# Performance work log

Hardware: AMD Instinct MI355X
Metric: run time of the kernel (lower is better)

Reference implementation:

```python
import jax, jax.numpy as jnp
import numpy as np

D_IN = 1024
D_OUT = 1024
NUM_HEADS = 16
HEAD_DIM = D_OUT // NUM_HEADS


def setup_inputs() -> dict:
    key = jax.random.key(0)
    ks = jax.random.split(key, 6)
    s = 0.02
    x = jax.random.normal(ks[0], (2, 2048, D_IN), dtype=jnp.float32)
    wq = jax.random.normal(ks[1], (D_IN, D_OUT), dtype=jnp.float32) * s
    wk = jax.random.normal(ks[2], (D_IN, D_OUT), dtype=jnp.float32) * s
    wv = jax.random.normal(ks[3], (D_IN, D_OUT), dtype=jnp.float32) * s
    wo = jax.random.normal(ks[4], (D_OUT, D_OUT), dtype=jnp.float32) * s
    bo = jax.random.normal(ks[5], (D_OUT,), dtype=jnp.float32) * s
    return {"x": x, "wq": wq, "wk": wk, "wv": wv, "wo": wo, "bo": bo}


def reference(x, wq, wk, wv, wo, bo):
    B, S, _ = x.shape
    # QKV projections (no bias, qkv_bias=False)
    def split_heads(t):
        return t.reshape(B, S, NUM_HEADS, HEAD_DIM).transpose(0, 2, 1, 3)  # [B,H,S,Dh]
    q = split_heads(x @ wq)
    k = split_heads(x @ wk)
    v = split_heads(x @ wv)
    scores = jnp.einsum('bhqd,bhkd->bhqk', q, k) / np.sqrt(HEAD_DIM).astype(np.float32)
    causal = jnp.tril(jnp.ones((S, S), dtype=bool))  # [S,S]
    scores = jnp.where(causal[None, None], scores, -jnp.inf)
    attn = jax.nn.softmax(scores, axis=-1)  # dropout p=0.0 -> identity
    ctx = jnp.einsum('bhqk,bhkd->bhqd', attn, v)
    ctx = ctx.transpose(0, 2, 1, 3).reshape(B, S, D_OUT)
    return ctx @ wo + bo
```

## Files before the change

kernel.cpp:

```cpp
#include <hip/hip_runtime.h>

typedef short s16x8 __attribute__((ext_vector_type(8)));
typedef float f32x4 __attribute__((ext_vector_type(4)));
typedef float f32x16 __attribute__((ext_vector_type(16)));
typedef unsigned int u32;
typedef u32 u32x2 __attribute__((ext_vector_type(2)));
typedef u32 u32x4 __attribute__((ext_vector_type(4)));
typedef unsigned short u16;

#define MFMA16(a, b, c) __builtin_amdgcn_mfma_f32_16x16x32_bf16((a), (b), (c), 0, 0, 0)
#define MFMA32(a, b, c) __builtin_amdgcn_mfma_f32_32x32x16_bf16((a), (b), (c), 0, 0, 0)

__device__ __forceinline__ u16 f2bf(float f) {
  unsigned u = __builtin_bit_cast(unsigned, f);
  unsigned r = (u + 0x7FFFu + ((u >> 16) & 1u)) >> 16;
  return (u16)r;
}

__device__ __forceinline__ u32 pack2bf(float lo, float hi) {
  return (u32)f2bf(lo) | ((u32)f2bf(hi) << 16);
}

__device__ __forceinline__ u32 cvtpk(float lo, float hi) {
  u32 r;
  asm("v_cvt_pk_bf16_f32 %0, %1, %2" : "=v"(r) : "v"(lo), "v"(hi));
  return r;
}

__device__ __forceinline__ float bf2f(u32 lo16) {
  return __builtin_bit_cast(float, lo16 << 16);
}

__device__ __forceinline__ void gl_lds16(const u16* g, u16* s) {
  __builtin_amdgcn_global_load_lds(
      (const __attribute__((address_space(1))) void*)g,
      (__attribute__((address_space(3))) void*)s, 16, 0, 0);
}

__global__ __launch_bounds__(256) void cvt_bf16(const float* __restrict__ in,
                                                u16* __restrict__ out, int n4) {
  int i = blockIdx.x * 256 + threadIdx.x;
  if (i < n4) {
    float4 v = reinterpret_cast<const float4*>(in)[i];
    ushort4 o;
    o.x = f2bf(v.x); o.y = f2bf(v.y); o.z = f2bf(v.z); o.w = f2bf(v.w);
    reinterpret_cast<ushort4*>(out)[i] = o;
  }
}

__global__ __launch_bounds__(256) void transp4(const float* __restrict__ wq,
                                               const float* __restrict__ wk,
                                               const float* __restrict__ wv,
                                               const float* __restrict__ wo,
                                               u16* __restrict__ wqkvt,
                                               u16* __restrict__ wot, float qscale) {
  __shared__ float tile[64][65];
  int z = blockIdx.z;
  const float* W = (z == 0) ? wq : (z == 1) ? wk : (z == 2) ? wv : wo;
  u16* out = (z < 3) ? (wqkvt + z * 1048576) : wot;
  float sc = (z == 0) ? qscale : 1.0f;
  int n0 = blockIdx.x * 64, k0 = blockIdx.y * 64;
  int t = threadIdx.x;
#pragma unroll
  for (int i = 0; i < 16; i++) {
    int idx = t + i * 256;
    int r = idx >> 6, c = idx & 63;
    tile[r][c] = W[(k0 + r) * 1024 + (n0 + c)];
  }
  __syncthreads();
#pragma unroll
  for (int i = 0; i < 16; i++) {
    int idx = t + i * 256;
    int r = idx >> 6, c = idx & 63;
    out[(n0 + r) * 1024 + (k0 + c)] = f2bf(tile[c][r] * sc);
  }
}

template <int MODE>
__global__ __launch_bounds__(256) void gemm2(const u16* __restrict__ A,
                                             const u16* __restrict__ Bt,
                                             const float* __restrict__ bias,
                                             void* __restrict__ outp) {
  constexpr int K = 1024, NT = K / 32;
  __shared__ __align__(16) u16 As[2][128 * 32];
  __shared__ __align__(16) u16 Bs[2][128 * 32];
  int t = threadIdx.x, w = t >> 6, l = t & 63;
  int m0 = blockIdx.y * 128, n0 = blockIdx.x * 128;
  int wm = (w >> 1) * 64, wn = (w & 1) * 64;
  int g = l >> 4, ql = l & 15;

  f32x4 acc[4][4];
#pragma unroll
  for (int i = 0; i < 4; i++)
#pragma unroll
    for (int j = 0; j < 4; j++) acc[i][j] = f32x4{0.f, 0.f, 0.f, 0.f};

  int lrow = l >> 2, lcol = (l & 3) * 8;
  const u16* Ag0 = A + (m0 + 32 * w + lrow) * K + lcol;
  const u16* Bg0 = Bt + (n0 + 32 * w + lrow) * K + lcol;
  u16* Asw[2] = {&As[0][(32 * w) * 32], &As[1][(32 * w) * 32]};
  u16* Bsw[2] = {&Bs[0][(32 * w) * 32], &Bs[1][(32 * w) * 32]};

#define STAGE(buf, kt)                              \
  do {                                              \
    int k0_ = (kt) * 32;                            \
    gl_lds16(Ag0 + k0_, Asw[buf]);                  \
    gl_lds16(Ag0 + 16 * K + k0_, Asw[buf] + 512);   \
    gl_lds16(Bg0 + k0_, Bsw[buf]);                  \
    gl_lds16(Bg0 + 16 * K + k0_, Bsw[buf] + 512);   \
  } while (0)

#define COMPUTE(buf)                                                              \
  do {                                                                            \
    s16x8 af[4], bv[4];                                                           \
    _Pragma("unroll") for (int fm = 0; fm < 4; fm++)                              \
        af[fm] = *reinterpret_cast<const s16x8*>(                                 \
            &As[buf][(wm + fm * 16 + ql) * 32 + g * 8]);                          \
    _Pragma("unroll") for (int fn = 0; fn < 4; fn++)                              \
        bv[fn] = *reinterpret_cast<const s16x8*>(                                 \
            &Bs[buf][(wn + fn * 16 + ql) * 32 + g * 8]);                          \
    _Pragma("unroll") for (int fm = 0; fm < 4; fm++)                              \
        _Pragma("unroll") for (int fn = 0; fn < 4; fn++)                          \
            acc[fm][fn] = MFMA16(af[fm], bv[fn], acc[fm][fn]);                    \
  } while (0)

  STAGE(0, 0);
  __syncthreads();
  int cur = 0;
  for (int kt = 0; kt < NT - 1; kt++) {
    STAGE(cur ^ 1, kt + 1);
    COMPUTE(cur);
    __syncthreads();
    cur ^= 1;
  }
  COMPUTE(cur);
#undef STAGE
#undef COMPUTE

#pragma unroll
  for (int fm = 0; fm < 4; fm++)
#pragma unroll
    for (int fn = 0; fn < 4; fn++)
#pragma unroll
      for (int j = 0; j < 4; j++) {
        int m = m0 + wm + fm * 16 + g * 4 + j;
        int n = n0 + wn + fn * 16 + ql;
        float v = acc[fm][fn][j];
        if (MODE == 0) {
          int proj = n >> 10, nn = n & 1023;
          int bh = (m >> 11) * 16 + (nn >> 6);
          int hd = nn & 63, srow = m & 2047;
          u16* o = (u16*)outp + proj * 4194304;
          if (proj < 2) {
            o[(bh * 2048 + srow) * 64 + hd] = f2bf(v);
          } else {
            int sp = (srow & ~12) | ((srow & 4) << 1) | ((srow & 8) >> 1);
            o[(bh * 64 + hd) * 2048 + sp] = f2bf(v);
          }
        } else {
          ((float*)outp)[m * 1024 + n] = v + bias[n];
        }
      }
}

__global__ __launch_bounds__(512, 4) void attn_kernel(const u16* __restrict__ Q,
                                                      const u16* __restrict__ Kb,
                                                      const u16* __restrict__ Vt,
                                                      u16* __restrict__ Ctx,
                                                      u16* __restrict__ part_o,
                                                      float* __restrict__ part_l) {
  __shared__ __align__(16) u16 Kl[2][2048];
  __shared__ __align__(16) u16 Vl[2][2048];
  __shared__ __align__(16) u16 tl[8][32 * 68];
  int tid = threadIdx.x, w = tid >> 6, l = tid & 63;
  int lq = l & 31, h = l >> 5;

  int B = blockIdx.x;
  int head = (B & 7) + 8 * ((B >> 3) & 3);
  int u = B >> 5;
  const signed char QCv[16] = {3, 2, 4, 4, 6, 6, 6, 7, 7, 7, 7, 5, 5, 5, 1, 0};
  const signed char CKv[16] = {0, 0, 0, 1, 0, 1, 2, 0, 1, 2, 3, 0, 1, 2, 0, 0};
  int qc = QCv[u], ck = CKv[u];
  int t0, t1;
  if (qc == 4)      { t0 = ck * 20; t1 = t0 + 20; }
  else if (qc == 5) { t0 = ck * 16; t1 = t0 + 16; }
  else if (qc == 6) { t0 = (ck == 0) ? 0 : (ck == 1) ? 19 : 38;
                      t1 = (ck == 0) ? 19 : (ck == 1) ? 38 : 56; }
  else if (qc == 7) { t0 = ck * 16; t1 = t0 + 16; }
  else              { t0 = 0; t1 = (qc + 1) * 8; }
  int dtile = qc * 8 + w;
  int q0w = qc * 256 + w * 32;
  int q = q0w + lq;

  const u16* Qp = Q + (head * 2048 + q0w) * 64;
  const u16* Kp = Kb + head * 2048 * 64;
  const u16* Vp = Vt + head * 64 * 2048;

  s16x8 qf[4];
#pragma unroll
  for (int f = 0; f < 4; f++)
    qf[f] = *reinterpret_cast<const s16x8*>(Qp + lq * 64 + f * 16 + h * 8);

  const u16* gstage;
  int gstep, ldsoff;
  if (w < 4) {
    int row = w * 8 + (l >> 3);
    int c = (l & 7) ^ (row & 7);
    gstage = Kp + row * 64 + c * 8;
    gstep = 32 * 64;
    ldsoff = w * 512;
  } else {
    int lin = (w - 4) * 64 + l;
    int rp = lin >> 3, pos = lin & 7;
    int d = rp * 2 + (pos >> 2);
    int c = (pos & 3) ^ (rp & 3);
    gstage = Vp + d * 2048 + c * 8;
    gstep = 32;
    ldsoff = (w - 4) * 512;
  }

  f32x16 oacc[2];
#pragma unroll
  for (int dt = 0; dt < 2; dt++)
#pragma unroll
    for (int rr = 0; rr < 16; rr++) oacc[dt][rr] = 0.f;
  float lsum = 0.f;

#define STAGE(buf, kt)                                                    \
  gl_lds16(gstage + (kt) * gstep, ((w < 4) ? Kl[buf] : Vl[buf]) + ldsoff)

  STAGE(0, t0);
  __syncthreads();
  int cur = 0;

  for (int kt = t0; kt < t1; kt++) {
    if (kt + 1 < t1) STAGE(cur ^ 1, kt + 1);

    if (kt <= dtile) {
      s16x8 kc[4];
#pragma unroll
      for (int f = 0; f < 4; f++)
        kc[f] = *reinterpret_cast<const s16x8*>(
            &Kl[cur][lq * 64 + (((f * 2 + h) ^ (lq & 7)) * 8)]);

      f32x16 s;
#pragma unroll
      for (int rr = 0; rr < 16; rr++) s[rr] = 0.f;
      __builtin_amdgcn_s_setprio(1);
#pragma unroll
      for (int f = 0; f < 4; f++) s = MFMA32(kc[f], qf[f], s);
      __builtin_amdgcn_s_setprio(0);

      float p[16];
      if (kt == dtile) {
        int kb = kt * 32;
#pragma unroll
        for (int rr = 0; rr < 16; rr++) {
          int key = kb + (rr & 3) + 8 * (rr >> 2) + 4 * h;
          float e = exp2f(s[rr]);
          p[rr] = (key <= q) ? e : 0.f;
        }
      } else {
#pragma unroll
        for (int rr = 0; rr < 16; rr++) p[rr] = exp2f(s[rr]);
      }
#pragma unroll
      for (int rr = 0; rr < 16; rr++) lsum += p[rr];

      u32 pw[2][4];
#pragma unroll
      for (int kh = 0; kh < 2; kh++)
#pragma unroll
        for (int uu = 0; uu < 4; uu++)
          pw[kh][uu] = cvtpk(p[kh * 8 + 2 * uu], p[kh * 8 + 2 * uu + 1]);

      s16x8 vf[2][2];
#pragma unroll
      for (int dt = 0; dt < 2; dt++)
#pragma unroll
        for (int kh = 0; kh < 2; kh++) {
          int rp = dt * 16 + (lq >> 1);
          int soff = rp * 64 + (lq & 1) * 32 + (((kh * 2 + h) ^ (rp & 3)) * 8);
          vf[dt][kh] = *reinterpret_cast<const s16x8*>(&Vl[cur][soff]);
        }

      __builtin_amdgcn_s_setprio(1);
#pragma unroll
      for (int kh = 0; kh < 2; kh++) {
        s16x8 pf = __builtin_bit_cast(
            s16x8, u32x4{pw[kh][0], pw[kh][1], pw[kh][2], pw[kh][3]});
        oacc[0] = MFMA32(vf[0][kh], pf, oacc[0]);
        oacc[1] = MFMA32(vf[1][kh], pf, oacc[1]);
      }
      __builtin_amdgcn_s_setprio(0);
    }

    __syncthreads();
    cur ^= 1;
  }
#undef STAGE

  if (qc >= 4) {
    int base = (qc == 4) ? 0 : (qc == 5) ? 2 : (qc == 6) ? 5 : 8;
    int rec = head * 12 + base + ck;
    u32* po = reinterpret_cast<u32*>(part_o) + (size_t)rec * 8192 + w * 1024 + l * 16;
#pragma unroll
    for (int dt = 0; dt < 2; dt++)
#pragma unroll
      for (int i = 0; i < 8; i++)
        po[dt * 8 + i] = pack2bf(oacc[dt][2 * i], oacc[dt][2 * i + 1]);
    part_l[(size_t)rec * 512 + w * 64 + l] = lsum;
    return;
  }

  float ltot = lsum + __shfl_xor(lsum, 32);
  float invl = 1.0f / ltot;
  u16* myl = tl[w];
#pragma unroll
  for (int dt = 0; dt < 2; dt++)
#pragma unroll
    for (int i = 0; i < 8; i++) {
      int d = ((2 * i) & 3) + 8 * (i >> 1) + 4 * h + dt * 32;
      u32 pkv = pack2bf(oacc[dt][2 * i] * invl, oacc[dt][2 * i + 1] * invl);
      *reinterpret_cast<u32*>(myl + lq * 68 + d) = pkv;
    }

  int b = head >> 4, hh = head & 15;
  int gbase = b * 2048 + q0w;
#pragma unroll
  for (int i = 0; i < 8; i++) {
    int chunkk = i * 64 + l;
    int row = chunkk >> 4, col4 = (chunkk & 15) * 4;
    u32x2 v = *reinterpret_cast<const u32x2*>(myl + row * 68 + col4);
    *reinterpret_cast<u32x2*>(Ctx + (gbase + row) * 1024 + hh * 64 + col4) = v;
  }
}

__global__ __launch_bounds__(256) void attn_combine(const u16* __restrict__ part_o,
                                                    const float* __restrict__ part_l,
                                                    u16* __restrict__ Ctx) {
  __shared__ __align__(16) u16 tl[4][32 * 68];
  int wv = threadIdx.x >> 6, l = threadIdx.x & 63;
  int lq = l & 31, h = l >> 5;
  int unit = blockIdx.x * 4 + wv;
  int head = unit & 31, rest = unit >> 5;
  int qc = 4 + (rest >> 3), w = rest & 7;
  int nc = (qc == 4) ? 2 : (qc == 7) ? 4 : 3;
  int base = (qc == 4) ? 0 : (qc == 5) ? 2 : (qc == 6) ? 5 : 8;
  int rec0 = head * 12 + base;

  float lsum = 0.f;
  float of[32];
#pragma unroll
  for (int i = 0; i < 32; i++) of[i] = 0.f;
  for (int cc = 0; cc < nc; cc++) {
    int rec = rec0 + cc;
    lsum += part_l[(size_t)rec * 512 + w * 64 + l];
    const u32* po =
        reinterpret_cast<const u32*>(part_o) + (size_t)rec * 8192 + w * 1024 + l * 16;
#pragma unroll
    for (int uu = 0; uu < 16; uu++) {
      u32 a = po[uu];
      of[2 * uu] += bf2f(a & 0xFFFFu);
      of[2 * uu + 1] += bf2f(a >> 16);
    }
  }

  float ltot = lsum + __shfl_xor(lsum, 32);
  float invl = 1.0f / ltot;

  u16* myl = tl[wv];
#pragma unroll
  for (int dt = 0; dt < 2; dt++)
#pragma unroll
    for (int i = 0; i < 8; i++) {
      int uu = dt * 8 + i;
      int d = ((2 * i) & 3) + 8 * (i >> 1) + 4 * h + dt * 32;
      *reinterpret_cast<u32*>(myl + lq * 68 + d) =
          pack2bf(of[2 * uu] * invl, of[2 * uu + 1] * invl);
    }

  int b_ = head >> 4, hh = head & 15;
  int gbase = b_ * 2048 + qc * 256 + w * 32;
#pragma unroll
  for (int i = 0; i < 8; i++) {
    int chunkk = i * 64 + l;
    int row = chunkk >> 4, col4 = (chunkk & 15) * 4;
    u32x2 v = *reinterpret_cast<const u32x2*>(myl + row * 68 + col4);
    *reinterpret_cast<u32x2*>(Ctx + (gbase + row) * 1024 + hh * 64 + col4) = v;
  }
}

extern "C" void kernel_launch(void* const* d_in, const int* in_sizes, int n_in,
                              void* d_out, int out_size, void* d_ws, size_t ws_size,
                              hipStream_t stream) {
  const float* x = (const float*)d_in[0];
  const float* wq = (const float*)d_in[1];
  const float* wk = (const float*)d_in[2];
  const float* wv = (const float*)d_in[3];
  const float* wo = (const float*)d_in[4];
  const float* bo = (const float*)d_in[5];

  char* ws = (char*)d_ws;
  const size_t MB = 1 << 20;
  u16* xb    = (u16*)(ws + 0 * MB);
  u16* wqkvt = (u16*)(ws + 8 * MB);
  u16* wot   = (u16*)(ws + 14 * MB);
  u16* qkv   = (u16*)(ws + 16 * MB);
  u16* ctx   = (u16*)(ws + 40 * MB);
  u16* part_o   = (u16*)(ws + 0 * MB);
  float* part_l = (float*)(ws + 12582912);

  const float QSCALE = 0.125f * 1.44269504f;

  cvt_bf16<<<4096, 256, 0, stream>>>(x, xb, 1048576);
  transp4<<<dim3(16, 16, 4), 256, 0, stream>>>(wq, wk, wv, wo, wqkvt, wot, QSCALE);

  gemm2<0><<<dim3(24, 32), 256, 0, stream>>>(xb, wqkvt, nullptr, qkv);

  attn_kernel<<<512, 512, 0, stream>>>(qkv, qkv + 4194304, qkv + 8388608, ctx,
                                       part_o, part_l);
  attn_combine<<<256, 256, 0, stream>>>(part_o, part_l, ctx);

  gemm2<1><<<dim3(8, 32), 256, 0, stream>>>(ctx, wot, bo, d_out);
}
```

Measured before the change: 122.1 us.

## Swizzle GEMM LDS tiles and stage QKV epilogue through LDS for vector stores

The GEMM's shared-memory tiles now use an XOR swizzle on the 8-element column chunk, on both the global-to-LDS staging and the fragment reads, to reduce bank conflicts. The QKV projection epilogue (MODE 0) now writes bf16 results into a per-wave LDS scratch area reused from the A tile buffer. It then reads them back and issues packed 8-byte global stores for Q/K rows and for the permuted, transposed V layout, instead of scattered 2-byte stores. This trades an extra barrier and LDS round trips for more coalesced global writes. Renaming the attention STAGE macro avoids a name clash.

```diff
diff --git a/kernel.cpp b/kernel.cpp
--- a/kernel.cpp
+++ b/kernel.cpp
@@ -88,6 +88,7 @@
   int m0 = blockIdx.y * 128, n0 = blockIdx.x * 128;
   int wm = (w >> 1) * 64, wn = (w & 1) * 64;
   int g = l >> 4, ql = l & 15;
+  int xs = (g ^ ((ql >> 1) & 3)) * 8;
 
   f32x4 acc[4][4];
 #pragma unroll
@@ -95,7 +96,7 @@
 #pragma unroll
     for (int j = 0; j < 4; j++) acc[i][j] = f32x4{0.f, 0.f, 0.f, 0.f};
 
-  int lrow = l >> 2, lcol = (l & 3) * 8;
+  int lrow = l >> 2, lcol = ((l & 3) ^ ((l >> 3) & 3)) * 8;
   const u16* Ag0 = A + (m0 + 32 * w + lrow) * K + lcol;
   const u16* Bg0 = Bt + (n0 + 32 * w + lrow) * K + lcol;
   u16* Asw[2] = {&As[0][(32 * w) * 32], &As[1][(32 * w) * 32]};
@@ -115,10 +116,10 @@
     s16x8 af[4], bv[4];                                                           \
     _Pragma("unroll") for (int fm = 0; fm < 4; fm++)                              \
         af[fm] = *reinterpret_cast<const s16x8*>(                                 \
-            &As[buf][(wm + fm * 16 + ql) * 32 + g * 8]);                          \
+            &As[buf][(wm + fm * 16 + ql) * 32 + xs]);                             \
     _Pragma("unroll") for (int fn = 0; fn < 4; fn++)                              \
         bv[fn] = *reinterpret_cast<const s16x8*>(                                 \
-            &Bs[buf][(wn + fn * 16 + ql) * 32 + g * 8]);                          \
+            &Bs[buf][(wn + fn * 16 + ql) * 32 + xs]);                             \
     _Pragma("unroll") for (int fm = 0; fm < 4; fm++)                              \
         _Pragma("unroll") for (int fn = 0; fn < 4; fn++)                          \
             acc[fm][fn] = MFMA16(af[fm], bv[fn], acc[fm][fn]);                    \
@@ -137,30 +138,72 @@
 #undef STAGE
 #undef COMPUTE
 
-#pragma unroll
-  for (int fm = 0; fm < 4; fm++)
-#pragma unroll
-    for (int fn = 0; fn < 4; fn++)
-#pragma unroll
-      for (int j = 0; j < 4; j++) {
-        int m = m0 + wm + fm * 16 + g * 4 + j;
-        int n = n0 + wn + fn * 16 + ql;
-        float v = acc[fm][fn][j];
-        if (MODE == 0) {
-          int proj = n >> 10, nn = n & 1023;
-          int bh = (m >> 11) * 16 + (nn >> 6);
-          int hd = nn & 63, srow = m & 2047;
-          u16* o = (u16*)outp + proj * 4194304;
-          if (proj < 2) {
-            o[(bh * 2048 + srow) * 64 + hd] = f2bf(v);
-          } else {
-            int sp = (srow & ~12) | ((srow & 4) << 1) | ((srow & 8) >> 1);
-            o[(bh * 64 + hd) * 2048 + sp] = f2bf(v);
-          }
-        } else {
-          ((float*)outp)[m * 1024 + n] = v + bias[n];
+  if (MODE == 1) {
+#pragma unroll
+    for (int fm = 0; fm < 4; fm++)
+#pragma unroll
+      for (int fn = 0; fn < 4; fn++)
+#pragma unroll
+        for (int j = 0; j < 4; j++) {
+          int m = m0 + wm + fm * 16 + g * 4 + j;
+          int n = n0 + wn + fn * 16 + ql;
+          ((float*)outp)[m * 1024 + n] = acc[fm][fn][j] + bias[n];
         }
+    return;
+  }
+
+  __syncthreads();
+  u16* tlw = &As[0][0] + w * 2048;
+  int nb = n0 + wn;
+  int proj = nb >> 10;
+  int nn6 = (nb & 1023) >> 6;
+
+  if (proj < 2) {
+    u16* o = (u16*)outp + proj * 4194304;
+#pragma unroll
+    for (int fm = 0; fm < 4; fm++) {
+#pragma unroll
+      for (int fn = 0; fn < 4; fn++)
+#pragma unroll
+        for (int j = 0; j < 4; j++)
+          tlw[(g * 4 + j) * 68 + fn * 16 + ql] = f2bf(acc[fm][fn][j]);
+#pragma unroll
+      for (int i = 0; i < 4; i++) {
+        int row = i * 4 + g;
+        u32x2 v = *reinterpret_cast<const u32x2*>(tlw + row * 68 + ql * 4);
+        int m = m0 + wm + fm * 16 + row;
+        int bh = (m >> 11) * 16 + nn6;
+        *reinterpret_cast<u32x2*>(o + (bh * 2048 + (m & 2047)) * 64 + ql * 4) = v;
       }
+    }
+  } else {
+    u16* o = (u16*)outp + 8388608;
+    int kq = (l & 3) * 4;
+    int pr = ((kq & 4) << 1) | ((kq & 8) >> 1);
+#pragma unroll
+    for (int fm = 0; fm < 4; fm++) {
+#pragma unroll
+      for (int fn = 0; fn < 4; fn++)
+#pragma unroll
+        for (int j = 0; j < 4; j++)
+          tlw[(g * 4 + j) * 68 + fn * 16 + ql] = f2bf(acc[fm][fn][j]);
+      int m = m0 + wm + fm * 16;
+      int batch = m >> 11, key0 = m & 2047;
+      int bh = batch * 16 + nn6;
+#pragma unroll
+      for (int i = 0; i < 4; i++) {
+        int hd = i * 16 + (l >> 2);
+        u16 v0 = tlw[(pr + 0) * 68 + hd];
+        u16 v1 = tlw[(pr + 1) * 68 + hd];
+        u16 v2 = tlw[(pr + 2) * 68 + hd];
+        u16 v3 = tlw[(pr + 3) * 68 + hd];
+        u32x2 v;
+        v[0] = (u32)v0 | ((u32)v1 << 16);
+        v[1] = (u32)v2 | ((u32)v3 << 16);
+        *reinterpret_cast<u32x2*>(o + (bh * 64 + hd) * 2048 + key0 + kq) = v;
+      }
+    }
+  }
 }
 
 __global__ __launch_bounds__(512, 4) void attn_kernel(const u16* __restrict__ Q,
@@ -226,15 +269,15 @@
     for (int rr = 0; rr < 16; rr++) oacc[dt][rr] = 0.f;
   float lsum = 0.f;
 
-#define STAGE(buf, kt)                                                    \
+#define STAGEKV(buf, kt)                                                  \
   gl_lds16(gstage + (kt) * gstep, ((w < 4) ? Kl[buf] : Vl[buf]) + ldsoff)
 
-  STAGE(0, t0);
+  STAGEKV(0, t0);
   __syncthreads();
   int cur = 0;
 
   for (int kt = t0; kt < t1; kt++) {
-    if (kt + 1 < t1) STAGE(cur ^ 1, kt + 1);
+    if (kt + 1 < t1) STAGEKV(cur ^ 1, kt + 1);
 
     if (kt <= dtile) {
       s16x8 kc[4];
@@ -298,7 +341,7 @@
     __syncthreads();
     cur ^= 1;
   }
-#undef STAGE
+#undef STAGEKV
 
   if (qc >= 4) {
     int base = (qc == 4) ? 0 : (qc == 5) ? 2 : (qc == 6) ? 5 : 8;
```

Result: no change. 122.0 us (-0.1%).
